# Kernel optimization log

Hardware: AMD Instinct MI355X
Metric: run time of the kernel (lower is better)

Reference implementation:

```python
import jax, jax.numpy as jnp
import numpy as np

EPS = 0.1        # entropic regularization
MAX_ITER = 50    # fixed iteration count (torch early-stops on host; we run all iters)
P = 1            # cost exponent
N_POINTS = 4096
D_FEAT = 2


def _cost_matrix(x, y):
    # x: [N, D], y: [M, D] -> C: [N, M], sum_d |x_i - y_j|^p
    return jnp.sum(jnp.abs(x[:, None, :] - y[None, :, :]) ** P, axis=-1)


def setup_inputs() -> dict:
    key = jax.random.key(0)
    k1, k2 = jax.random.split(key)
    x = jax.random.normal(k1, (N_POINTS, D_FEAT), dtype=jnp.float32)
    y = jax.random.normal(k2, (N_POINTS, D_FEAT), dtype=jnp.float32)
    return {"x": x, "y": y}


def reference(x, y):
    n, m = x.shape[0], y.shape[0]
    C = _cost_matrix(x, y)  # [N, M]
    log_mu = jnp.log(jnp.full((n,), 1.0 / n, dtype=x.dtype) + 1e-8)
    log_nu = jnp.log(jnp.full((m,), 1.0 / m, dtype=y.dtype) + 1e-8)

    def M(u, v):
        # modified cost: (-C + u_i + v_j) / eps
        return (-C + u[:, None] + v[None, :]) / EPS

    def step(carry, _):
        u, v = carry
        u = EPS * (log_mu - jax.scipy.special.logsumexp(M(u, v), axis=-1)) + u
        v = EPS * (log_nu - jax.scipy.special.logsumexp(M(u, v), axis=-2)) + v
        return (u, v), None

    u0 = jnp.zeros((n,), dtype=x.dtype)
    v0 = jnp.zeros((m,), dtype=y.dtype)
    (u, v), _ = jax.lax.scan(step, (u0, v0), None, length=MAX_ITER)

    pi = jnp.exp(M(u, v))                 # transport plan [N, M]
    cost = jnp.sum(pi * C)                # scalar (reduction='none', 2D input)
    return cost ** (1.0 / P), pi, C
```

## Files before the change

kernel.cpp:

```cpp
#include <hip/hip_runtime.h>


#define NPTS    4096
#define EPS_F   0.1f
#define S_L2E   14.426950408889634f
#define INV_SL  0.0693147180559945f
#define A_LOGMU (-0.8317725207f)
#define N_ITER  50
#define NBLK    256
#define TPB     1024
#define WPB     (TPB / 64)
#define RPW     2
#define HALFC   2048
#define NJT     (HALFC / 256)
#define NLEAF   16
#define BSTRIDE 64
#define BAR_INTS ((NLEAF + 1 + NLEAF) * BSTRIDE)

typedef float f4u __attribute__((ext_vector_type(4), aligned(4)));

__device__ __forceinline__ float fexp2(float x) {
#if __has_builtin(__builtin_amdgcn_exp2f)
  return __builtin_amdgcn_exp2f(x);
#else
  float r;
  asm("v_exp_f32 %0, %1" : "=v"(r) : "v"(x));
  return r;
#endif
}

__device__ __forceinline__ float coh_load(const float* p) {
  return __hip_atomic_load(p, __ATOMIC_RELAXED, __HIP_MEMORY_SCOPE_AGENT);
}
__device__ __forceinline__ void coh_store(float* p, float x) {
  __hip_atomic_store(p, x, __ATOMIC_RELAXED, __HIP_MEMORY_SCOPE_AGENT);
}

__device__ __forceinline__ float wave_sum64(float x) {
#pragma unroll
  for (int off = 32; off > 0; off >>= 1) x += __shfl_xor(x, off, 64);
  return x;
}

__device__ __forceinline__ void grid_barrier(int* bar, int k) {
  __syncthreads();
  if (threadIdx.x == 0) {
    const int myleaf = blockIdx.x & (NLEAF - 1);
    int* leaf = bar + myleaf * BSTRIDE;
    const int old = __hip_atomic_fetch_add(leaf, 1, __ATOMIC_RELAXED,
                                           __HIP_MEMORY_SCOPE_AGENT);
    if (old == NLEAF * k - 1)
      __hip_atomic_store(bar + (NLEAF + 1 + myleaf) * BSTRIDE, k,
                         __ATOMIC_RELAXED, __HIP_MEMORY_SCOPE_AGENT);
    for (;;) {
      int mn = k;
#pragma unroll
      for (int rr = 0; rr < NLEAF; ++rr) {
        const int f = __hip_atomic_load(bar + (NLEAF + 1 + rr) * BSTRIDE,
                                        __ATOMIC_RELAXED,
                                        __HIP_MEMORY_SCOPE_AGENT);
        mn = min(mn, f);
      }
      if (mn >= k) break;
      __builtin_amdgcn_s_sleep(1);
    }
  }
  __syncthreads();
}

__device__ __forceinline__ void stageW(const float* __restrict__ win,
                                       float* __restrict__ sW, int tid) {
  const int c = tid * 4;
  const float w0 = coh_load(win + c + 0), w1 = coh_load(win + c + 1);
  const float w2 = coh_load(win + c + 2), w3 = coh_load(win + c + 3);
  float4 W;
  W.x = w0 * S_L2E;  W.y = w1 * S_L2E;  W.z = w2 * S_L2E;  W.w = w3 * S_L2E;
  *(float4*)(sW + c) = W;
  __syncthreads();
}

__device__ __forceinline__ void stageCoords(const float* __restrict__ colp,
                                            float* __restrict__ sC0,
                                            float* __restrict__ sC1, int tid) {
  const int c = tid * 4;
  const float4 a = ((const float4*)colp)[(c >> 1) + 0];
  const float4 b = ((const float4*)colp)[(c >> 1) + 1];
  float4 C0, C1;
  C0.x = a.x * S_L2E; C0.y = a.z * S_L2E; C0.z = b.x * S_L2E; C0.w = b.z * S_L2E;
  C1.x = a.y * S_L2E; C1.y = a.w * S_L2E; C1.z = b.y * S_L2E; C1.w = b.w * S_L2E;
  *(float4*)(sC0 + c) = C0;
  *(float4*)(sC1 + c) = C1;
}

__device__ __forceinline__ void phaseU(const float* __restrict__ sW,
                                       const float (&Dreg)[NJT][RPW][4],
                                       float (*sPart)[RPW],
                                       float* __restrict__ wout,
                                       int row0blk, int wv, int lane, int tid,
                                       int base) {
  float acc0 = 0.f, acc1 = 0.f;
#pragma unroll
  for (int jt = 0; jt < NJT; ++jt) {
    const int j = base + jt * 256;
    const float4 W = *(const float4*)(sW + j);
    acc0 += (fexp2(W.x - Dreg[jt][0][0]) + fexp2(W.y - Dreg[jt][0][1])) +
            (fexp2(W.z - Dreg[jt][0][2]) + fexp2(W.w - Dreg[jt][0][3]));
    acc1 += (fexp2(W.x - Dreg[jt][1][0]) + fexp2(W.y - Dreg[jt][1][1])) +
            (fexp2(W.z - Dreg[jt][1][2]) + fexp2(W.w - Dreg[jt][1][3]));
  }
  const float S0 = wave_sum64(acc0);
  const float S1 = wave_sum64(acc1);
  if (lane == 0) { sPart[wv][0] = S0; sPart[wv][1] = S1; }
  __syncthreads();
  if (tid < 16) {
    const int p = tid >> 1, r = tid & 1;
    const float S = sPart[2 * p][r] + sPart[2 * p + 1][r];
    coh_store(wout + row0blk + p * RPW + r, A_LOGMU - EPS_F * __logf(S));
  }
}

__device__ __forceinline__ void phaseV(const float* __restrict__ rx,
                                       const float* __restrict__ ry,
                                       const float* __restrict__ sW,
                                       const float* __restrict__ sC0,
                                       const float* __restrict__ sC1,
                                       float (*sPart)[RPW],
                                       float* __restrict__ wout,
                                       int row0blk, int wv, int lane, int tid,
                                       int base) {
  float acc0 = 0.f, acc1 = 0.f;
#pragma unroll
  for (int jt = 0; jt < NJT; ++jt) {
    const int j = base + jt * 256;
    const float4 W  = *(const float4*)(sW + j);
    const float4 C0 = *(const float4*)(sC0 + j);
    const float4 C1 = *(const float4*)(sC1 + j);
    {
      const float a0 = (W.x - fabsf(rx[0] - C0.x)) - fabsf(ry[0] - C1.x);
      const float a1 = (W.y - fabsf(rx[0] - C0.y)) - fabsf(ry[0] - C1.y);
      const float a2 = (W.z - fabsf(rx[0] - C0.z)) - fabsf(ry[0] - C1.z);
      const float a3 = (W.w - fabsf(rx[0] - C0.w)) - fabsf(ry[0] - C1.w);
      acc0 += (fexp2(a0) + fexp2(a1)) + (fexp2(a2) + fexp2(a3));
    }
    {
      const float a0 = (W.x - fabsf(rx[1] - C0.x)) - fabsf(ry[1] - C1.x);
      const float a1 = (W.y - fabsf(rx[1] - C0.y)) - fabsf(ry[1] - C1.y);
      const float a2 = (W.z - fabsf(rx[1] - C0.z)) - fabsf(ry[1] - C1.z);
      const float a3 = (W.w - fabsf(rx[1] - C0.w)) - fabsf(ry[1] - C1.w);
      acc1 += (fexp2(a0) + fexp2(a1)) + (fexp2(a2) + fexp2(a3));
    }
  }
  const float S0 = wave_sum64(acc0);
  const float S1 = wave_sum64(acc1);
  if (lane == 0) { sPart[wv][0] = S0; sPart[wv][1] = S1; }
  __syncthreads();
  if (tid < 16) {
    const int p = tid >> 1, r = tid & 1;
    const float S = sPart[2 * p][r] + sPart[2 * p + 1][r];
    coh_store(wout + row0blk + p * RPW + r, A_LOGMU - EPS_F * __logf(S));
  }
}

__global__ void __launch_bounds__(TPB, 4)
sinkhorn_main(const float* __restrict__ x, const float* __restrict__ y,
              float* __restrict__ u, float* __restrict__ v,
              float* __restrict__ out, int* __restrict__ bar) {
  __shared__ float sW[NPTS];
  __shared__ float sC0y[NPTS], sC1y[NPTS];
  __shared__ float sC0x[NPTS], sC1x[NPTS];
  __shared__ float sPart[WPB][RPW];
  __shared__ float sCost[WPB];

  const int tid  = threadIdx.x;
  const int wv   = tid >> 6;
  const int lane = tid & 63;
  const int row0blk = blockIdx.x * (WPB / 2) * RPW;
  const int row0 = row0blk + (wv >> 1) * RPW;
  const int base = (wv & 1) * HALFC + lane * 4;

  float rxu[RPW], ryu[RPW], rxv[RPW], ryv[RPW];
#pragma unroll
  for (int r = 0; r < RPW; ++r) {
    const float2 xr = ((const float2*)x)[row0 + r];
    const float2 yr = ((const float2*)y)[row0 + r];
    rxu[r] = xr.x * S_L2E;  ryu[r] = xr.y * S_L2E;
    rxv[r] = yr.x * S_L2E;  ryv[r] = yr.y * S_L2E;
  }

  stageCoords(y, sC0y, sC1y, tid);
  stageCoords(x, sC0x, sC1x, tid);
  __syncthreads();

  float Dreg[NJT][RPW][4];
#pragma unroll
  for (int jt = 0; jt < NJT; ++jt) {
    const int j = base + jt * 256;
    const float4 C0 = *(const float4*)(sC0y + j);
    const float4 C1 = *(const float4*)(sC1y + j);
#pragma unroll
    for (int r = 0; r < RPW; ++r) {
      Dreg[jt][r][0] = fabsf(rxu[r] - C0.x) + fabsf(ryu[r] - C1.x);
      Dreg[jt][r][1] = fabsf(rxu[r] - C0.y) + fabsf(ryu[r] - C1.y);
      Dreg[jt][r][2] = fabsf(rxu[r] - C0.z) + fabsf(ryu[r] - C1.z);
      Dreg[jt][r][3] = fabsf(rxu[r] - C0.w) + fabsf(ryu[r] - C1.w);
    }
  }

  int k = 0;
  for (int it = 0; it < N_ITER; ++it) {
    stageW(v, sW, tid);
    phaseU(sW, Dreg, sPart, u, row0blk, wv, lane, tid, base);
    grid_barrier(bar, ++k);
    stageW(u, sW, tid);
    phaseV(rxv, ryv, sW, sC0x, sC1x, sPart, v, row0blk, wv, lane, tid, base);
    grid_barrier(bar, ++k);
  }
  stageW(v, sW, tid);

  float* __restrict__ pi = out + 1;
  float* __restrict__ cm = out + 1 + (size_t)NPTS * NPTS;
  float uu[RPW];
#pragma unroll
  for (int r = 0; r < RPW; ++r) uu[r] = coh_load(u + row0 + r) * S_L2E;

  float costacc = 0.f;
#pragma unroll
  for (int jt = 0; jt < NJT; ++jt) {
    const int j = base + jt * 256;
    const float4 W = *(const float4*)(sW + j);
#pragma unroll
    for (int r = 0; r < RPW; ++r) {
      const float s0 = Dreg[jt][r][0];
      const float s1 = Dreg[jt][r][1];
      const float s2 = Dreg[jt][r][2];
      const float s3 = Dreg[jt][r][3];
      const float p0 = fexp2((uu[r] + W.x) - s0);
      const float p1 = fexp2((uu[r] + W.y) - s1);
      const float p2 = fexp2((uu[r] + W.z) - s2);
      const float p3 = fexp2((uu[r] + W.w) - s3);
      costacc = fmaf(p0, s0, costacc);
      costacc = fmaf(p1, s1, costacc);
      costacc = fmaf(p2, s2, costacc);
      costacc = fmaf(p3, s3, costacc);
      const size_t off = (size_t)(row0 + r) * NPTS + j;
      f4u pv; pv.x = p0; pv.y = p1; pv.z = p2; pv.w = p3;
      f4u cv; cv.x = s0 * INV_SL; cv.y = s1 * INV_SL;
      cv.z = s2 * INV_SL; cv.w = s3 * INV_SL;
      *(f4u*)(pi + off) = pv;
      *(f4u*)(cm + off) = cv;
    }
  }
  const float cw = wave_sum64(costacc);
  if (lane == 0) sCost[wv] = cw;
  __syncthreads();
  if (tid == 0) {
    float c = 0.f;
#pragma unroll
    for (int w = 0; w < WPB; ++w) c += sCost[w];
    atomicAdd(out, c * INV_SL);
  }
}

__global__ void sinkhorn_init(float* __restrict__ v, int* __restrict__ bar,
                              float* __restrict__ out) {
  const int i = blockIdx.x * blockDim.x + threadIdx.x;
  if (i < NPTS) coh_store(v + i, 0.f);
  if (i < BAR_INTS)
    __hip_atomic_store(bar + i, 0, __ATOMIC_RELAXED, __HIP_MEMORY_SCOPE_AGENT);
  if (i == 0) out[0] = 0.f;
}

extern "C" void kernel_launch(void* const* d_in, const int* in_sizes, int n_in,
                              void* d_out, int out_size, void* d_ws, size_t ws_size,
                              hipStream_t stream) {
  const float* x = (const float*)d_in[0];
  const float* y = (const float*)d_in[1];
  float* u = (float*)d_ws;
  float* v = u + NPTS;
  int* bar = (int*)(v + NPTS);
  float* out = (float*)d_out;

  sinkhorn_init<<<dim3(16), dim3(256), 0, stream>>>(v, bar, out);

  void* args[6];
  args[0] = (void*)&x;
  args[1] = (void*)&y;
  args[2] = (void*)&u;
  args[3] = (void*)&v;
  args[4] = (void*)&out;
  args[5] = (void*)&bar;
  hipLaunchCooperativeKernel((void*)sinkhorn_main, dim3(NBLK), dim3(TPB),
                             args, 0, stream);
}
```

Baseline: 688.5 us.

## Split each row's columns across two blocks with partial-sum exchange

Adds a new cooperative kernel that runs 512 blocks, each handling 16 rows over half the columns, with one row per wave. Blocks write raw partial sums, and the log/potential is computed while staging the next phase, which removes the in-block cross-wave reduction. Occupancy is doubled to two blocks per CU. In exchange, the cost terms are recomputed instead of cached in registers, and twice as many blocks take part in the grid barrier. An occupancy query picks the old kernel as a fallback when two blocks cannot fit per CU.

New measurement: 695.4 us. No clear change (+1.0%).

```diff
diff --git a/kernel.cpp b/kernel.cpp
--- a/kernel.cpp
+++ b/kernel.cpp
@@ -7,12 +7,6 @@
 #define INV_SL  0.0693147180559945f
 #define A_LOGMU (-0.8317725207f)
 #define N_ITER  50
-#define NBLK    256
-#define TPB     1024
-#define WPB     (TPB / 64)
-#define RPW     2
-#define HALFC   2048
-#define NJT     (HALFC / 256)
 #define NLEAF   16
 #define BSTRIDE 64
 #define BAR_INTS ((NLEAF + 1 + NLEAF) * BSTRIDE)
@@ -42,14 +36,14 @@
   return x;
 }
 
-__device__ __forceinline__ void grid_barrier(int* bar, int k) {
+__device__ __forceinline__ void grid_barrier(int* bar, int k, int arrpl) {
   __syncthreads();
   if (threadIdx.x == 0) {
     const int myleaf = blockIdx.x & (NLEAF - 1);
-    int* leaf = bar + myleaf * BSTRIDE;
-    const int old = __hip_atomic_fetch_add(leaf, 1, __ATOMIC_RELAXED,
+    const int old = __hip_atomic_fetch_add(bar + myleaf * BSTRIDE, 1,
+                                           __ATOMIC_RELAXED,
                                            __HIP_MEMORY_SCOPE_AGENT);
-    if (old == NLEAF * k - 1)
+    if (old == arrpl * k - 1)
       __hip_atomic_store(bar + (NLEAF + 1 + myleaf) * BSTRIDE, k,
                          __ATOMIC_RELAXED, __HIP_MEMORY_SCOPE_AGENT);
     for (;;) {
@@ -67,6 +61,137 @@
   }
   __syncthreads();
 }
+
+#define SBLK  512
+#define STPB  1024
+#define SARR  (SBLK / NLEAF)
+#define SCOLS 2048
+
+__device__ __forceinline__ void stage_half(
+    const float* __restrict__ part, const float* __restrict__ colp,
+    float* __restrict__ sW, float* __restrict__ sC0, float* __restrict__ sC1,
+    int tid, int colbase, bool zero) {
+  const int c2 = tid * 2;
+  const int g = colbase + c2;
+  const float4 a = ((const float4*)colp)[g >> 1];
+  float w0 = 0.f, w1 = 0.f;
+  if (!zero) {
+    const float p00 = coh_load(part + g), p01 = coh_load(part + g + 1);
+    const float p10 = coh_load(part + NPTS + g);
+    const float p11 = coh_load(part + NPTS + g + 1);
+    w0 = (A_LOGMU - EPS_F * __logf(p00 + p10)) * S_L2E;
+    w1 = (A_LOGMU - EPS_F * __logf(p01 + p11)) * S_L2E;
+  }
+  float2 W, C0, C1;
+  W.x = w0;            W.y = w1;
+  C0.x = a.x * S_L2E;  C0.y = a.z * S_L2E;
+  C1.x = a.y * S_L2E;  C1.y = a.w * S_L2E;
+  *(float2*)(sW + c2)  = W;
+  *(float2*)(sC0 + c2) = C0;
+  *(float2*)(sC1 + c2) = C1;
+  __syncthreads();
+}
+
+__device__ __forceinline__ void phase_half(
+    const float rx, const float ry, const float* __restrict__ sW,
+    const float* __restrict__ sC0, const float* __restrict__ sC1,
+    float* __restrict__ pout, int half, int row, int lane) {
+  float acc = 0.f;
+#pragma unroll
+  for (int jt = 0; jt < 8; ++jt) {
+    const int j = lane * 4 + jt * 256;
+    const float4 W  = *(const float4*)(sW + j);
+    const float4 C0 = *(const float4*)(sC0 + j);
+    const float4 C1 = *(const float4*)(sC1 + j);
+    const float a0 = (W.x - fabsf(rx - C0.x)) - fabsf(ry - C1.x);
+    const float a1 = (W.y - fabsf(rx - C0.y)) - fabsf(ry - C1.y);
+    const float a2 = (W.z - fabsf(rx - C0.z)) - fabsf(ry - C1.z);
+    const float a3 = (W.w - fabsf(rx - C0.w)) - fabsf(ry - C1.w);
+    acc += (fexp2(a0) + fexp2(a1)) + (fexp2(a2) + fexp2(a3));
+  }
+  const float S = wave_sum64(acc);
+  if (lane == 0) coh_store(pout + half * NPTS + row, S);
+}
+
+__global__ void __launch_bounds__(STPB, 8)
+sinkhorn_split(const float* __restrict__ x, const float* __restrict__ y,
+               float* __restrict__ pu, float* __restrict__ pv,
+               float* __restrict__ out, int* __restrict__ bar) {
+  __shared__ float sW[SCOLS], sC0[SCOLS], sC1[SCOLS];
+  __shared__ float sCost[16];
+
+  const int tid  = threadIdx.x;
+  const int wv   = tid >> 6;
+  const int lane = tid & 63;
+  const int half = blockIdx.x & 1;
+  const int colbase = half * SCOLS;
+  const int row  = (blockIdx.x >> 1) * 16 + wv;
+
+  const float2 xr = ((const float2*)x)[row];
+  const float2 yr = ((const float2*)y)[row];
+  const float rxu = xr.x * S_L2E, ryu = xr.y * S_L2E;
+  const float rxv = yr.x * S_L2E, ryv = yr.y * S_L2E;
+
+  int k = 0;
+  for (int it = 0; it < N_ITER; ++it) {
+    stage_half(pv, y, sW, sC0, sC1, tid, colbase, it == 0);
+    phase_half(rxu, ryu, sW, sC0, sC1, pu, half, row, lane);
+    grid_barrier(bar, ++k, SARR);
+    stage_half(pu, x, sW, sC0, sC1, tid, colbase, false);
+    phase_half(rxv, ryv, sW, sC0, sC1, pv, half, row, lane);
+    grid_barrier(bar, ++k, SARR);
+  }
+  stage_half(pv, y, sW, sC0, sC1, tid, colbase, false);
+
+  float* __restrict__ pi = out + 1;
+  float* __restrict__ cm = out + 1 + (size_t)NPTS * NPTS;
+  const float su = coh_load(pu + row) + coh_load(pu + NPTS + row);
+  const float uu = (A_LOGMU - EPS_F * __logf(su)) * S_L2E;
+
+  float costacc = 0.f;
+#pragma unroll 2
+  for (int jt = 0; jt < 8; ++jt) {
+    const int j = lane * 4 + jt * 256;
+    const float4 W  = *(const float4*)(sW + j);
+    const float4 C0 = *(const float4*)(sC0 + j);
+    const float4 C1 = *(const float4*)(sC1 + j);
+    const float s0 = fabsf(rxu - C0.x) + fabsf(ryu - C1.x);
+    const float s1 = fabsf(rxu - C0.y) + fabsf(ryu - C1.y);
+    const float s2 = fabsf(rxu - C0.z) + fabsf(ryu - C1.z);
+    const float s3 = fabsf(rxu - C0.w) + fabsf(ryu - C1.w);
+    const float p0 = fexp2((uu + W.x) - s0);
+    const float p1 = fexp2((uu + W.y) - s1);
+    const float p2 = fexp2((uu + W.z) - s2);
+    const float p3 = fexp2((uu + W.w) - s3);
+    costacc = fmaf(p0, s0, costacc);
+    costacc = fmaf(p1, s1, costacc);
+    costacc = fmaf(p2, s2, costacc);
+    costacc = fmaf(p3, s3, costacc);
+    const size_t off = (size_t)row * NPTS + colbase + j;
+    f4u pvv; pvv.x = p0; pvv.y = p1; pvv.z = p2; pvv.w = p3;
+    f4u cv;  cv.x = s0 * INV_SL; cv.y = s1 * INV_SL;
+    cv.z = s2 * INV_SL; cv.w = s3 * INV_SL;
+    *(f4u*)(pi + off) = pvv;
+    *(f4u*)(cm + off) = cv;
+  }
+  const float cw = wave_sum64(costacc);
+  if (lane == 0) sCost[wv] = cw;
+  __syncthreads();
+  if (tid == 0) {
+    float c = 0.f;
+#pragma unroll
+    for (int w = 0; w < 16; ++w) c += sCost[w];
+    atomicAdd(out, c * INV_SL);
+  }
+}
+
+#define FBLK  256
+#define FTPB  1024
+#define WPB   (FTPB / 64)
+#define RPW   2
+#define HALFC 2048
+#define NJT   (HALFC / 256)
+#define FARR  (FBLK / NLEAF)
 
 __device__ __forceinline__ void stageW(const float* __restrict__ win,
                                        float* __restrict__ sW, int tid) {
@@ -92,12 +217,12 @@
   *(float4*)(sC1 + c) = C1;
 }
 
-__device__ __forceinline__ void phaseU(const float* __restrict__ sW,
-                                       const float (&Dreg)[NJT][RPW][4],
-                                       float (*sPart)[RPW],
-                                       float* __restrict__ wout,
-                                       int row0blk, int wv, int lane, int tid,
-                                       int base) {
+__device__ __forceinline__ void fb_phaseU(const float* __restrict__ sW,
+                                          const float (&Dreg)[NJT][RPW][4],
+                                          float (*sPart)[RPW],
+                                          float* __restrict__ wout,
+                                          int row0blk, int wv, int lane,
+                                          int tid, int base) {
   float acc0 = 0.f, acc1 = 0.f;
 #pragma unroll
   for (int jt = 0; jt < NJT; ++jt) {
@@ -119,15 +244,15 @@
   }
 }
 
-__device__ __forceinline__ void phaseV(const float* __restrict__ rx,
-                                       const float* __restrict__ ry,
-                                       const float* __restrict__ sW,
-                                       const float* __restrict__ sC0,
-                                       const float* __restrict__ sC1,
-                                       float (*sPart)[RPW],
-                                       float* __restrict__ wout,
-                                       int row0blk, int wv, int lane, int tid,
-                                       int base) {
+__device__ __forceinline__ void fb_phaseV(const float* __restrict__ rx,
+                                          const float* __restrict__ ry,
+                                          const float* __restrict__ sW,
+                                          const float* __restrict__ sC0,
+                                          const float* __restrict__ sC1,
+                                          float (*sPart)[RPW],
+                                          float* __restrict__ wout,
+                                          int row0blk, int wv, int lane,
+                                          int tid, int base) {
   float acc0 = 0.f, acc1 = 0.f;
 #pragma unroll
   for (int jt = 0; jt < NJT; ++jt) {
@@ -161,10 +286,10 @@
   }
 }
 
-__global__ void __launch_bounds__(TPB, 4)
-sinkhorn_main(const float* __restrict__ x, const float* __restrict__ y,
-              float* __restrict__ u, float* __restrict__ v,
-              float* __restrict__ out, int* __restrict__ bar) {
+__global__ void __launch_bounds__(FTPB, 4)
+sinkhorn_fallback(const float* __restrict__ x, const float* __restrict__ y,
+                  float* __restrict__ u, float* __restrict__ v,
+                  float* __restrict__ out, int* __restrict__ bar) {
   __shared__ float sW[NPTS];
   __shared__ float sC0y[NPTS], sC1y[NPTS];
   __shared__ float sC0x[NPTS], sC1x[NPTS];
@@ -209,11 +334,11 @@
   int k = 0;
   for (int it = 0; it < N_ITER; ++it) {
     stageW(v, sW, tid);
-    phaseU(sW, Dreg, sPart, u, row0blk, wv, lane, tid, base);
-    grid_barrier(bar, ++k);
+    fb_phaseU(sW, Dreg, sPart, u, row0blk, wv, lane, tid, base);
+    grid_barrier(bar, ++k, FARR);
     stageW(u, sW, tid);
-    phaseV(rxv, ryv, sW, sC0x, sC1x, sPart, v, row0blk, wv, lane, tid, base);
-    grid_barrier(bar, ++k);
+    fb_phaseV(rxv, ryv, sW, sC0x, sC1x, sPart, v, row0blk, wv, lane, tid, base);
+    grid_barrier(bar, ++k, FARR);
   }
   stageW(v, sW, tid);
 
@@ -243,10 +368,10 @@
       costacc = fmaf(p2, s2, costacc);
       costacc = fmaf(p3, s3, costacc);
       const size_t off = (size_t)(row0 + r) * NPTS + j;
-      f4u pv; pv.x = p0; pv.y = p1; pv.z = p2; pv.w = p3;
-      f4u cv; cv.x = s0 * INV_SL; cv.y = s1 * INV_SL;
+      f4u pvv; pvv.x = p0; pvv.y = p1; pvv.z = p2; pvv.w = p3;
+      f4u cv;  cv.x = s0 * INV_SL; cv.y = s1 * INV_SL;
       cv.z = s2 * INV_SL; cv.w = s3 * INV_SL;
-      *(f4u*)(pi + off) = pv;
+      *(f4u*)(pi + off) = pvv;
       *(f4u*)(cm + off) = cv;
     }
   }
@@ -261,34 +386,45 @@
   }
 }
 
-__global__ void sinkhorn_init(float* __restrict__ v, int* __restrict__ bar,
+__global__ void sinkhorn_init(float* __restrict__ buf, int* __restrict__ bar,
                               float* __restrict__ out) {
   const int i = blockIdx.x * blockDim.x + threadIdx.x;
-  if (i < NPTS) coh_store(v + i, 0.f);
+  if (i < 4 * NPTS) coh_store(buf + i, 0.f);
   if (i < BAR_INTS)
     __hip_atomic_store(bar + i, 0, __ATOMIC_RELAXED, __HIP_MEMORY_SCOPE_AGENT);
   if (i == 0) out[0] = 0.f;
 }
 
 extern "C" void kernel_launch(void* const* d_in, const int* in_sizes, int n_in,
-                              void* d_out, int out_size, void* d_ws, size_t ws_size,
-                              hipStream_t stream) {
+                              void* d_out, int out_size, void* d_ws,
+                              size_t ws_size, hipStream_t stream) {
   const float* x = (const float*)d_in[0];
   const float* y = (const float*)d_in[1];
-  float* u = (float*)d_ws;
-  float* v = u + NPTS;
-  int* bar = (int*)(v + NPTS);
+  float* pu = (float*)d_ws;
+  float* pv = pu + 2 * NPTS;
+  int* bar = (int*)(pv + 2 * NPTS);
   float* out = (float*)d_out;
 
-  sinkhorn_init<<<dim3(16), dim3(256), 0, stream>>>(v, bar, out);
-
-  void* args[6];
-  args[0] = (void*)&x;
-  args[1] = (void*)&y;
-  args[2] = (void*)&u;
-  args[3] = (void*)&v;
-  args[4] = (void*)&out;
-  args[5] = (void*)&bar;
-  hipLaunchCooperativeKernel((void*)sinkhorn_main, dim3(NBLK), dim3(TPB),
-                             args, 0, stream);
-}
+  sinkhorn_init<<<dim3(64), dim3(256), 0, stream>>>(pu, bar, out);
+
+  int maxb = 0;
+  hipOccupancyMaxActiveBlocksPerMultiprocessor(&maxb, sinkhorn_split, STPB, 0);
+
+  if (maxb >= 2) {
+    void* args[6];
+    args[0] = (void*)&x;  args[1] = (void*)&y;
+    args[2] = (void*)&pu; args[3] = (void*)&pv;
+    args[4] = (void*)&out; args[5] = (void*)&bar;
+    hipLaunchCooperativeKernel((void*)sinkhorn_split, dim3(SBLK), dim3(STPB),
+                               args, 0, stream);
+  } else {
+    float* u = pu;
+    float* v = pv;
+    void* args[6];
+    args[0] = (void*)&x;  args[1] = (void*)&y;
+    args[2] = (void*)&u;  args[3] = (void*)&v;
+    args[4] = (void*)&out; args[5] = (void*)&bar;
+    hipLaunchCooperativeKernel((void*)sinkhorn_fallback, dim3(FBLK),
+                               dim3(FTPB), args, 0, stream);
+  }
+}
```
